# Performance work log

Measured on AMD Instinct MI355X. Metric: run time of the kernel, lower is better.

## Reference

```python
import jax, jax.numpy as jnp
import numpy as np

L = 3          # num_layer
D = 128        # emb_dim
N_INST = 40000
N_NET = 10000
N = N_INST + N_NET
E = 800000
EPS = 1e-5


def setup_inputs() -> dict:
    key = jax.random.key(0)
    ks = jax.random.split(key, 16)
    g = lambda k, shape: jax.random.normal(k, shape, jnp.float32) * 0.05
    return {
        'x': jax.random.normal(ks[0], (N_INST, 11), jnp.float32),
        'x_net': jax.random.normal(ks[1], (N_NET, 3), jnp.float32),
        # encoder for instance nodes: 11 -> 2D -> D
        'enc_W1': g(ks[2], (2 * D, 11)), 'enc_b1': jnp.zeros((2 * D,), jnp.float32),
        'enc_W2': g(ks[3], (D, 2 * D)), 'enc_b2': jnp.zeros((D,), jnp.float32),
        # encoder for net nodes: 3 -> D -> D
        'encn_W1': g(ks[4], (D, 3)), 'encn_b1': jnp.zeros((D,), jnp.float32),
        'encn_W2': g(ks[5], (D, D)), 'encn_b2': jnp.zeros((D,), jnp.float32),
        # forward-direction GCN convs
        'conv_W': g(ks[6], (L, D, D)), 'conv_b': jnp.zeros((L, D), jnp.float32),
        'conv_root': g(ks[7], (L, D)),
        # reverse-direction GCN convs
        'rconv_W': g(ks[8], (L, D, D)), 'rconv_b': jnp.zeros((L, D), jnp.float32),
        'rconv_root': g(ks[9], (L, D)),
        # layernorms
        'ln_g': jnp.ones((L, D), jnp.float32), 'ln_b': jnp.zeros((L, D), jnp.float32),
        # graph edge list
        'src': jax.random.randint(ks[10], (E,), 0, N, jnp.int32),
        'dst': jax.random.randint(ks[11], (E,), 0, N, jnp.int32),
        'num_instances': N_INST,
    }


def _lrelu(v):
    return jnp.where(v >= 0, v, 0.1 * v)


def _gcn_conv(h, W, b, root, e_src, e_dst, deg, dinv):
    # h: [N, D]; e_src/e_dst: [E]; deg/dinv: [N]
    x = h @ W.T + b                                   # [N, D]
    norm = dinv[e_src] * dinv[e_dst]                  # [E]
    msg = norm[:, None] * jax.nn.relu(x[e_src])       # [E, D] gather + scale
    agg = jax.ops.segment_sum(msg, e_dst, num_segments=N)  # [N, D] scatter-add
    self_loop = jax.nn.relu(x + root) / deg[:, None]
    return agg + self_loop


def reference(x, x_net, enc_W1, enc_b1, enc_W2, enc_b2,
              encn_W1, encn_b1, encn_W2, encn_b2,
              conv_W, conv_b, conv_root, rconv_W, rconv_b, rconv_root,
              ln_g, ln_b, src, dst, num_instances):
    # node encoders
    h_inst = _lrelu(_lrelu(x @ enc_W1.T + enc_b1) @ enc_W2.T + enc_b2)
    h_net = _lrelu(_lrelu(x_net @ encn_W1.T + encn_b1) @ encn_W2.T + encn_b2)
    h = jnp.concatenate([h_inst, h_net], axis=0)      # [N, D]

    ones = jnp.ones((E,), jnp.float32)
    deg_in = jax.ops.segment_sum(ones, dst, num_segments=N) + 1.0
    deg_out = jax.ops.segment_sum(ones, src, num_segments=N) + 1.0
    dinv_in = jnp.where(jnp.isinf(deg_in ** -0.5), 0.0, deg_in ** -0.5)
    dinv_out = jnp.where(jnp.isinf(deg_out ** -0.5), 0.0, deg_out ** -0.5)

    h_list = [h]
    for l in range(L):
        hf = _gcn_conv(h, conv_W[l], conv_b[l], conv_root[l], src, dst, deg_in, dinv_in)
        # reverse graph: edges flipped -> src/dst swapped, degrees swap roles
        hr = _gcn_conv(h, rconv_W[l], rconv_b[l], rconv_root[l], dst, src, deg_out, dinv_out)
        s = hf + hr
        mu = jnp.mean(s, axis=-1, keepdims=True)
        var = jnp.mean((s - mu) ** 2, axis=-1, keepdims=True)
        s = (s - mu) * jax.lax.rsqrt(var + EPS) * ln_g[l] + ln_b[l]
        s = _lrelu(s)
        h = s + h  # residual
        h_list.append(h)

    rep = jnp.concatenate(h_list, axis=1)             # [N, (L+1)*D] (JK='concat')
    return rep[num_instances:]                        # net-node representations
```

## Files before the change

kernel.cpp:

```cpp
#include <hip/hip_runtime.h>
#include <hip/hip_bf16.h>


constexpr int D = 128;
constexpr int CAP = 48;

typedef float f32x4 __attribute__((ext_vector_type(4)));
typedef float f32x2 __attribute__((ext_vector_type(2)));
typedef __bf16 bf16x8v __attribute__((ext_vector_type(8)));

#if defined(__has_builtin)
# if __has_builtin(__builtin_amdgcn_cvt_pk_f32_fp8) && __has_builtin(__builtin_amdgcn_cvt_pk_fp8_f32)
#  define HAS_HW_FP8 1
# endif
#endif
#ifndef HAS_HW_FP8
# define HAS_HW_FP8 0
#endif

__device__ __forceinline__ unsigned short f2bf(float f) {
    unsigned u = __float_as_uint(f);
    unsigned r = (u + 0x7fffu + ((u >> 16) & 1u)) >> 16;
    return (unsigned short)r;
}
__device__ __forceinline__ float bflo(unsigned u) { return __uint_as_float(u << 16); }
__device__ __forceinline__ float bfhi(unsigned u) { return __uint_as_float(u & 0xffff0000u); }

__device__ __forceinline__ unsigned enc_fp8_1(float f) {
    unsigned u = __float_as_uint(f);
    u += 0x7FFFFu + ((u >> 20) & 1u);
    int e = (int)(u >> 23) - 120;
    unsigned m = (u >> 20) & 7u;
    if (e <= 0) return 0u;
    if (e > 15 || (e == 15 && m == 7u)) return 0x7Eu;
    return ((unsigned)e << 3) | m;
}
__device__ __forceinline__ unsigned pack_fp8x2(float a, float b) {
#if HAS_HW_FP8
    return (unsigned)__builtin_amdgcn_cvt_pk_fp8_f32(a, b, 0, false) & 0xFFFFu;
#else
    return enc_fp8_1(a) | (enc_fp8_1(b) << 8);
#endif
}
__device__ __forceinline__ float dec_fp8_1(unsigned b) {
    unsigned e = (b >> 3) & 0xFu, m = b & 7u;
    unsigned bits = ((e + 120u) << 23) | (m << 20);
    return e ? __uint_as_float(bits) : 0.0f;
}
__device__ __forceinline__ void dec_fp8x4(unsigned u, float o[4]) {
#if HAS_HW_FP8
    f32x2 lo = __builtin_amdgcn_cvt_pk_f32_fp8((int)u, false);
    f32x2 hi = __builtin_amdgcn_cvt_pk_f32_fp8((int)u, true);
    o[0] = lo.x; o[1] = lo.y; o[2] = hi.x; o[3] = hi.y;
#else
    o[0] = dec_fp8_1(u & 0xFF); o[1] = dec_fp8_1((u >> 8) & 0xFF);
    o[2] = dec_fp8_1((u >> 16) & 0xFF); o[3] = dec_fp8_1(u >> 24);
#endif
}

__global__ __launch_bounds__(256) void prep_kernel(
    const float* __restrict__ cW, const float* __restrict__ rW,
    const float* __restrict__ eW2, const float* __restrict__ enW2,
    unsigned short* __restrict__ cWb, unsigned short* __restrict__ rWb,
    unsigned short* __restrict__ eW2b, unsigned short* __restrict__ enW2b,
    int* __restrict__ cnt_i, int* __restrict__ cnt_o,
    int ncw, int nrw, int new2, int nenw2, int N)
{
    int i = blockIdx.x * 256 + threadIdx.x;
    if (i < ncw) { cWb[i] = f2bf(cW[i]); return; }
    i -= ncw;
    if (i < nrw) { rWb[i] = f2bf(rW[i]); return; }
    i -= nrw;
    if (i < new2) { eW2b[i] = f2bf(eW2[i]); return; }
    i -= new2;
    if (i < nenw2) { enW2b[i] = f2bf(enW2[i]); return; }
    i -= nenw2;
    if (i < N) { cnt_i[i] = 0; return; }
    i -= N;
    if (i < N) { cnt_o[i] = 0; }
}

__global__ __launch_bounds__(256) void fill_part(
    const int* __restrict__ src, const int* __restrict__ dst, int E,
    int* __restrict__ cnt_i, int* __restrict__ cnt_o,
    unsigned short* __restrict__ slot_i, unsigned short* __restrict__ slot_o,
    int N, int prange, int chunk)
{
    int part = blockIdx.x & 7;
    int slice = blockIdx.x >> 3;
    int lo = part * prange, hi = min(N, lo + prange);
    int e0 = slice * chunk, e1 = min(E, e0 + chunk);
    for (int e = e0 + (int)threadIdx.x * 4; e < e1; e += 1024) {
        int4 s4 = *(const int4*)(src + e);
        int4 d4 = *(const int4*)(dst + e);
        int ss[4] = {s4.x, s4.y, s4.z, s4.w};
        int dd[4] = {d4.x, d4.y, d4.z, d4.w};
        #pragma unroll
        for (int j = 0; j < 4; ++j) {
            int d = dd[j], s = ss[j];
            if (d >= lo && d < hi) {
                int p = atomicAdd(&cnt_i[d], 1);
                if (p < CAP) slot_i[(size_t)d * CAP + p] = (unsigned short)s;
            }
            if (s >= lo && s < hi) {
                int p = atomicAdd(&cnt_o[s], 1);
                if (p < CAP) slot_o[(size_t)s * CAP + p] = (unsigned short)d;
            }
        }
    }
}

__global__ __launch_bounds__(256) void enc_gemm1(
    const float* __restrict__ x, const float* __restrict__ x_net,
    const float* __restrict__ W1, const float* __restrict__ b1,
    const float* __restrict__ Wn1, const float* __restrict__ bn1,
    unsigned short* __restrict__ t1, unsigned short* __restrict__ t2,
    int NI, int NN, int nbi)
{
    int b = blockIdx.x;
    const float *A, *W, *bias; unsigned short* Cb;
    int M, K, OUT, ldc, bx, by;
    if (b < nbi * 4) {
        bx = b >> 2; by = b & 3;
        A = x; W = W1; bias = b1; Cb = t1; M = NI; K = 11; OUT = 256; ldc = 256;
    } else {
        b -= nbi * 4;
        bx = b >> 1; by = b & 1;
        A = x_net; W = Wn1; bias = bn1; Cb = t2; M = NN; K = 3; OUT = 128; ldc = 128;
    }
    __shared__ __align__(16) float As[16][68];
    __shared__ __align__(16) float Ws[16][68];
    int row0 = bx * 64, col0 = by * 64;
    int t = threadIdx.x;
    int tx = t & 15, ty = t >> 4;
    float acc[4][4] = {};
    {
        #pragma unroll
        for (int i = 0; i < 4; ++i) {
            int e = t + i * 256;
            int m = e >> 4, k = e & 15;
            int gr = row0 + m;
            As[k][m] = (gr < M && k < K) ? A[(size_t)gr * K + k] : 0.f;
            int gn = col0 + m;
            Ws[k][m] = (gn < OUT && k < K) ? W[(size_t)gn * K + k] : 0.f;
        }
        __syncthreads();
        #pragma unroll
        for (int k = 0; k < 16; ++k) {
            float4 av = *(const float4*)&As[k][ty * 4];
            float4 bv = *(const float4*)&Ws[k][tx * 4];
            float a[4] = {av.x, av.y, av.z, av.w};
            float bb[4] = {bv.x, bv.y, bv.z, bv.w};
            #pragma unroll
            for (int ii = 0; ii < 4; ++ii)
                #pragma unroll
                for (int jj = 0; jj < 4; ++jj)
                    acc[ii][jj] = fmaf(a[ii], bb[jj], acc[ii][jj]);
        }
    }
    #pragma unroll
    for (int ii = 0; ii < 4; ++ii) {
        int gr = row0 + ty * 4 + ii;
        if (gr >= M) continue;
        #pragma unroll
        for (int jj = 0; jj < 4; ++jj) {
            int gn = col0 + tx * 4 + jj;
            if (gn >= OUT) continue;
            float v = acc[ii][jj] + bias[gn];
            v = (v >= 0.f) ? v : 0.1f * v;
            Cb[(size_t)gr * ldc + gn] = f2bf(v);
        }
    }
}

__device__ __forceinline__ void mfma_core(
    const unsigned short* __restrict__ A, const unsigned short* __restrict__ W,
    int M, int K, int row0, int lane, f32x4 acc[8])
{
    int arc = min(row0 + (lane & 15), M - 1);
    int kq = (lane >> 4) * 8;
    const unsigned short* arow = A + (size_t)arc * K + kq;
    const unsigned short* wbase = W + (size_t)(lane & 15) * K + kq;
    for (int k0 = 0; k0 < K; k0 += 32) {
        bf16x8v a = *reinterpret_cast<const bf16x8v*>(arow + k0);
        #pragma unroll
        for (int j = 0; j < 8; ++j) {
            bf16x8v b = *reinterpret_cast<const bf16x8v*>(wbase + (size_t)j * 16 * K + k0);
            acc[j] = __builtin_amdgcn_mfma_f32_16x16x32_bf16(a, b, acc[j], 0, 0, 0);
        }
    }
}

__global__ __launch_bounds__(256) void enc_gemm2(
    const unsigned short* __restrict__ t1, const unsigned short* __restrict__ t2,
    const unsigned short* __restrict__ W2b, const unsigned short* __restrict__ Wn2b,
    const float* __restrict__ b2, const float* __restrict__ bn2,
    float* __restrict__ h, unsigned short* __restrict__ hb,
    float* __restrict__ out, int NI, int NN, int nbi)
{
    int b = blockIdx.x;
    const unsigned short *A, *W; const float* bias;
    int M, K; bool isnet;
    int wave = threadIdx.x >> 6;
    int lane = threadIdx.x & 63;
    int row0;
    if (b < nbi) {
        A = t1; W = W2b; bias = b2; M = NI; K = 256; isnet = false;
        row0 = b * 64 + wave * 16;
    } else {
        A = t2; W = Wn2b; bias = bn2; M = NN; K = 128; isnet = true;
        row0 = (b - nbi) * 64 + wave * 16;
    }
    f32x4 acc[8];
    #pragma unroll
    for (int j = 0; j < 8; ++j) acc[j] = (f32x4){0.f, 0.f, 0.f, 0.f};
    mfma_core(A, W, M, K, row0, lane, acc);
    int cbase = lane & 15;
    int rsub = (lane >> 4) * 4;
    #pragma unroll
    for (int j = 0; j < 8; ++j) {
        int f = j * 16 + cbase;
        float bv = bias[f];
        #pragma unroll
        for (int q = 0; q < 4; ++q) {
            int r = row0 + rsub + q;
            if (r >= M) continue;
            float v = acc[j][q] + bv;
            v = (v >= 0.f) ? v : 0.1f * v;
            int gr = isnet ? NI + r : r;
            h[(size_t)gr * D + f] = v;
            hb[(size_t)gr * D + f] = f2bf(v);
            if (isnet) out[(size_t)r * 512 + f] = v;
        }
    }
}

__global__ __launch_bounds__(256) void conv_gemm(
    const unsigned short* __restrict__ hb,
    const unsigned short* __restrict__ Wf, const unsigned short* __restrict__ Wr,
    const float* __restrict__ biasf, const float* __restrict__ biasr,
    const float* __restrict__ rootf, const float* __restrict__ rootr,
    const int* __restrict__ cnt_i, const int* __restrict__ cnt_o,
    unsigned char* __restrict__ mf, unsigned char* __restrict__ mr,
    unsigned short* __restrict__ sl, int M)
{
    int wave = threadIdx.x >> 6;
    int lane = threadIdx.x & 63;
    int row0 = blockIdx.x * 64 + wave * 16;
    f32x4 accf[8], accr[8];
    #pragma unroll
    for (int j = 0; j < 8; ++j) {
        accf[j] = (f32x4){0.f, 0.f, 0.f, 0.f};
        accr[j] = (f32x4){0.f, 0.f, 0.f, 0.f};
    }
    int arc = min(row0 + (lane & 15), M - 1);
    int kq = (lane >> 4) * 8;
    const unsigned short* arow = hb + (size_t)arc * D + kq;
    const unsigned short* wfb = Wf + (size_t)(lane & 15) * D + kq;
    const unsigned short* wrb = Wr + (size_t)(lane & 15) * D + kq;
    for (int k0 = 0; k0 < D; k0 += 32) {
        bf16x8v a = *reinterpret_cast<const bf16x8v*>(arow + k0);
        #pragma unroll
        for (int j = 0; j < 8; ++j) {
            bf16x8v bf_ = *reinterpret_cast<const bf16x8v*>(wfb + (size_t)j * 16 * D + k0);
            accf[j] = __builtin_amdgcn_mfma_f32_16x16x32_bf16(a, bf_, accf[j], 0, 0, 0);
        }
        #pragma unroll
        for (int j = 0; j < 8; ++j) {
            bf16x8v br_ = *reinterpret_cast<const bf16x8v*>(wrb + (size_t)j * 16 * D + k0);
            accr[j] = __builtin_amdgcn_mfma_f32_16x16x32_bf16(a, br_, accr[j], 0, 0, 0);
        }
    }
    int cbase = lane & 15;
    int rsub = (lane >> 4) * 4;
    float di[4], dou[4], rdi[4], rdo[4];
    #pragma unroll
    for (int q = 0; q < 4; ++q) {
        int r = min(row0 + rsub + q, M - 1);
        float ci = (float)cnt_i[r] + 1.0f;
        float co = (float)cnt_o[r] + 1.0f;
        di[q] = rsqrtf(ci) * 64.0f; rdi[q] = 1.0f / ci;
        dou[q] = rsqrtf(co) * 64.0f; rdo[q] = 1.0f / co;
    }
    #pragma unroll
    for (int j = 0; j < 8; j += 2) {
        int f0 = j * 16 + cbase, f1 = f0 + 16;
        float bf0 = biasf[f0], bf1 = biasf[f1];
        float br0 = biasr[f0], br1 = biasr[f1];
        float rf0 = rootf[f0], rf1 = rootf[f1];
        float rr0 = rootr[f0], rr1 = rootr[f1];
        #pragma unroll
        for (int q = 0; q < 4; ++q) {
            int r = row0 + rsub + q;
            if (r >= M) continue;
            float vf0 = accf[j][q] + bf0, vf1 = accf[j + 1][q] + bf1;
            float vr0 = accr[j][q] + br0, vr1 = accr[j + 1][q] + br1;
            size_t o0 = (size_t)r * D + f0, o1 = (size_t)r * D + f1;
            unsigned em = pack_fp8x2(di[q] * fmaxf(vf0, 0.f), di[q] * fmaxf(vf1, 0.f));
            mf[o0] = (unsigned char)(em & 0xFF);
            mf[o1] = (unsigned char)(em >> 8);
            unsigned er = pack_fp8x2(dou[q] * fmaxf(vr0, 0.f), dou[q] * fmaxf(vr1, 0.f));
            mr[o0] = (unsigned char)(er & 0xFF);
            mr[o1] = (unsigned char)(er >> 8);
            sl[o0] = f2bf(fmaxf(vf0 + rf0, 0.f) * rdi[q] + fmaxf(vr0 + rr0, 0.f) * rdo[q]);
            sl[o1] = f2bf(fmaxf(vf1 + rf1, 0.f) * rdi[q] + fmaxf(vr1 + rr1, 0.f) * rdo[q]);
        }
    }
}

__device__ __forceinline__ void gather_dir(
    const unsigned char* __restrict__ m, const unsigned short* __restrict__ lst,
    int sn, int lane, int rl, size_t fb, float a[4])
{
    int idx = (lane < sn) ? (int)lst[lane] : 0;
    int k = 0;
    for (; k + 8 <= sn; k += 8) {
        int p0 = __shfl(idx, k + rl);
        int p1 = __shfl(idx, k + 2 + rl);
        int p2 = __shfl(idx, k + 4 + rl);
        int p3 = __shfl(idx, k + 6 + rl);
        unsigned u0 = *(const unsigned*)(m + (((size_t)p0) << 7) + fb);
        unsigned u1 = *(const unsigned*)(m + (((size_t)p1) << 7) + fb);
        unsigned u2 = *(const unsigned*)(m + (((size_t)p2) << 7) + fb);
        unsigned u3 = *(const unsigned*)(m + (((size_t)p3) << 7) + fb);
        float t0[4], t1[4], t2[4], t3[4];
        dec_fp8x4(u0, t0); dec_fp8x4(u1, t1); dec_fp8x4(u2, t2); dec_fp8x4(u3, t3);
        a[0] += t0[0] + t1[0] + t2[0] + t3[0];
        a[1] += t0[1] + t1[1] + t2[1] + t3[1];
        a[2] += t0[2] + t1[2] + t2[2] + t3[2];
        a[3] += t0[3] + t1[3] + t2[3] + t3[3];
    }
    for (; k + 2 <= sn; k += 2) {
        int p = __shfl(idx, k + rl);
        unsigned u = *(const unsigned*)(m + (((size_t)p) << 7) + fb);
        float t[4];
        dec_fp8x4(u, t);
        a[0] += t[0]; a[1] += t[1]; a[2] += t[2]; a[3] += t[3];
    }
    if (k < sn) {
        int p = __shfl(idx, k);
        if (rl == 0) {
            unsigned u = *(const unsigned*)(m + (((size_t)p) << 7) + fb);
            float t[4];
            dec_fp8x4(u, t);
            a[0] += t[0]; a[1] += t[1]; a[2] += t[2]; a[3] += t[3];
        }
    }
}

__global__ __launch_bounds__(256) void agg_kernel(
    const unsigned char* __restrict__ mf, const unsigned char* __restrict__ mr,
    const unsigned short* __restrict__ sl,
    float* __restrict__ h, unsigned short* __restrict__ hb,
    const int* __restrict__ cnt_i, const unsigned short* __restrict__ slot_i,
    const int* __restrict__ cnt_o, const unsigned short* __restrict__ slot_o,
    const float* __restrict__ g, const float* __restrict__ bta,
    float* __restrict__ out, int N, int NI, int layer)
{
    int wid = (blockIdx.x * blockDim.x + threadIdx.x) >> 6;
    if (wid >= N) return;
    int lane = threadIdx.x & 63;
    int fl = lane & 31;
    int rl = lane >> 5;
    size_t fb = (size_t)fl * 4;

    int ci_raw = cnt_i[wid], co_raw = cnt_o[wid];
    int sni = min(ci_raw, CAP), sno = min(co_raw, CAP);

    float a[4] = {0.f, 0.f, 0.f, 0.f};
    float b[4] = {0.f, 0.f, 0.f, 0.f};
    gather_dir(mf, slot_i + (size_t)wid * CAP, sni, lane, rl, fb, a);
    gather_dir(mr, slot_o + (size_t)wid * CAP, sno, lane, rl, fb, b);

    #pragma unroll
    for (int j = 0; j < 4; ++j) {
        a[j] += __shfl_xor(a[j], 32);
        b[j] += __shfl_xor(b[j], 32);
    }
    int half = lane >> 1;
    float ta0 = __shfl(a[0], half), ta1 = __shfl(a[1], half);
    float ta2 = __shfl(a[2], half), ta3 = __shfl(a[3], half);
    float tb0 = __shfl(b[0], half), tb1 = __shfl(b[1], half);
    float tb2 = __shfl(b[2], half), tb3 = __shfl(b[3], half);
    float ga0 = (lane & 1) ? ta2 : ta0;
    float ga1 = (lane & 1) ? ta3 : ta1;
    float gb0 = (lane & 1) ? tb2 : tb0;
    float gb1 = (lane & 1) ? tb3 : tb1;

    int d0 = lane * 2;
    float di = rsqrtf((float)ci_raw + 1.0f) * 0.015625f;
    float dou = rsqrtf((float)co_raw + 1.0f) * 0.015625f;
    unsigned usl = *(const unsigned*)(sl + (((size_t)wid) << 7) + d0);
    float s_0 = di * ga0 + dou * gb0 + bflo(usl);
    float s_1 = di * ga1 + dou * gb1 + bfhi(usl);

    float sm = s_0 + s_1;
    float sq = s_0 * s_0 + s_1 * s_1;
    #pragma unroll
    for (int o = 32; o >= 1; o >>= 1) {
        sm += __shfl_xor(sm, o);
        sq += __shfl_xor(sq, o);
    }
    float mu = sm * (1.0f / 128.0f);
    float var = sq * (1.0f / 128.0f) - mu * mu;
    float rs = rsqrtf(var + 1e-5f);

    float2 gv = *(const float2*)(g + d0);
    float2 bv = *(const float2*)(bta + d0);
    float2 hv = *(const float2*)(h + (((size_t)wid) << 7) + d0);
    float y0 = (s_0 - mu) * rs * gv.x + bv.x;
    float y1 = (s_1 - mu) * rs * gv.y + bv.y;
    y0 = (y0 >= 0.f) ? y0 : 0.1f * y0;
    y1 = (y1 >= 0.f) ? y1 : 0.1f * y1;
    y0 += hv.x; y1 += hv.y;
    *(float2*)(h + (((size_t)wid) << 7) + d0) = make_float2(y0, y1);
    if (layer < 2) {
        unsigned packed = (unsigned)f2bf(y0) | ((unsigned)f2bf(y1) << 16);
        *(unsigned*)(hb + (((size_t)wid) << 7) + d0) = packed;
    }
    if (wid >= NI) {
        *(float2*)(out + (size_t)(wid - NI) * 512 + (size_t)(layer + 1) * 128 + d0) = make_float2(y0, y1);
    }
}

static inline int cdiv(int a, int b) { return (a + b - 1) / b; }

extern "C" void kernel_launch(void* const* d_in, const int* in_sizes, int n_in,
                              void* d_out, int out_size, void* d_ws, size_t ws_size,
                              hipStream_t stream)
{
    const float* x        = (const float*)d_in[0];
    const float* x_net    = (const float*)d_in[1];
    const float* enc_W1   = (const float*)d_in[2];
    const float* enc_b1   = (const float*)d_in[3];
    const float* enc_W2   = (const float*)d_in[4];
    const float* enc_b2   = (const float*)d_in[5];
    const float* encn_W1  = (const float*)d_in[6];
    const float* encn_b1  = (const float*)d_in[7];
    const float* encn_W2  = (const float*)d_in[8];
    const float* encn_b2  = (const float*)d_in[9];
    const float* conv_W   = (const float*)d_in[10];
    const float* conv_b   = (const float*)d_in[11];
    const float* conv_root= (const float*)d_in[12];
    const float* rconv_W  = (const float*)d_in[13];
    const float* rconv_b  = (const float*)d_in[14];
    const float* rconv_root=(const float*)d_in[15];
    const float* ln_g     = (const float*)d_in[16];
    const float* ln_b     = (const float*)d_in[17];
    const int*   src      = (const int*)d_in[18];
    const int*   dst      = (const int*)d_in[19];

    const int NI = in_sizes[0] / 11;
    const int NN = in_sizes[1] / 3;
    const int N  = NI + NN;
    const int E  = in_sizes[18];
    float* out = (float*)d_out;

    char* ws = (char*)d_ws;
    size_t offq = 0;
    auto alloc = [&](size_t bytes) -> void* {
        void* p = ws + offq;
        offq += (bytes + 255) & ~(size_t)255;
        return p;
    };
    float*          h    = (float*)alloc((size_t)N * D * 4);
    unsigned short* hb   = (unsigned short*)alloc((size_t)N * D * 2);
    unsigned char*  mf   = (unsigned char*)alloc((size_t)N * D);
    unsigned char*  mr   = (unsigned char*)alloc((size_t)N * D);
    unsigned short* sl   = (unsigned short*)alloc((size_t)N * D * 2);
    unsigned short* tmp2b = (unsigned short*)alloc((size_t)NN * D * 2);
    unsigned short* slot_i = (unsigned short*)alloc((size_t)N * CAP * 2);
    unsigned short* slot_o = (unsigned short*)alloc((size_t)N * CAP * 2);
    int*   cnt_i  = (int*)alloc((size_t)N * 4);
    int*   cnt_o  = (int*)alloc((size_t)N * 4);
    unsigned short* encW2b  = (unsigned short*)alloc((size_t)in_sizes[4] * 2);
    unsigned short* encnW2b = (unsigned short*)alloc((size_t)in_sizes[8] * 2);
    unsigned short* convWb  = (unsigned short*)alloc((size_t)in_sizes[10] * 2);
    unsigned short* rconvWb = (unsigned short*)alloc((size_t)in_sizes[13] * 2);
    unsigned short* tmp1b = (unsigned short*)mf;

    const int ncw = in_sizes[10], nrw = in_sizes[13];
    const int new2 = in_sizes[4], nenw2 = in_sizes[8];
    int prep_total = ncw + nrw + new2 + nenw2 + 2 * N;
    prep_kernel<<<cdiv(prep_total, 256), 256, 0, stream>>>(
        conv_W, rconv_W, enc_W2, encn_W2, convWb, rconvWb, encW2b, encnW2b,
        cnt_i, cnt_o, ncw, nrw, new2, nenw2, N);

    const int prange = cdiv(N, 8);
    const int chunk = 4096;
    const int NS = cdiv(E, chunk);
    fill_part<<<8 * NS, 256, 0, stream>>>(src, dst, E, cnt_i, cnt_o,
                                          slot_i, slot_o, N, prange, chunk);

    const int nbi1 = cdiv(NI, 64);
    const int nbn1 = cdiv(NN, 64);
    enc_gemm1<<<nbi1 * 4 + nbn1 * 2, 256, 0, stream>>>(
        x, x_net, enc_W1, enc_b1, encn_W1, encn_b1, tmp1b, tmp2b, NI, NN, nbi1);
    enc_gemm2<<<nbi1 + nbn1, 256, 0, stream>>>(
        tmp1b, tmp2b, encW2b, encnW2b, enc_b2, encn_b2, h, hb, out, NI, NN, nbi1);

    for (int l = 0; l < 3; ++l) {
        conv_gemm<<<cdiv(N, 64), 256, 0, stream>>>(
            hb, convWb + (size_t)l * D * D, rconvWb + (size_t)l * D * D,
            conv_b + (size_t)l * D, rconv_b + (size_t)l * D,
            conv_root + (size_t)l * D, rconv_root + (size_t)l * D,
            cnt_i, cnt_o, mf, mr, sl, N);
        agg_kernel<<<cdiv(N * 64, 256), 256, 0, stream>>>(
            mf, mr, sl, h, hb, cnt_i, slot_i, cnt_o, slot_o,
            ln_g + (size_t)l * D, ln_b + (size_t)l * D,
            out, N, NI, l);
    }
}
```

Measured before the change: 413.0 us.

## Fuse all stages into one cooperative persistent kernel with grid syncs

Replaces the sequence of separate kernel launches (prep, fill, two encoder GEMMs, per-layer conv and aggregation) with a single cooperative persistent kernel that loops over tiles and separates stages with grid-wide syncs. The aim is to remove launch gaps and tail effects between the many short stages. The conv GEMM tile also changes to 32 rows, with waves split across column halves, and fp8 packing becomes per-element. The cost is grid-sync overhead, occupancy limits from the 256x4 launch bounds, and fill/encoder work now sharing one phase. A fallback path with separate launches is kept.

```diff
diff --git a/kernel.cpp b/kernel.cpp
--- a/kernel.cpp
+++ b/kernel.cpp
@@ -1,5 +1,8 @@
 #include <hip/hip_runtime.h>
 #include <hip/hip_bf16.h>
+#include <hip/hip_cooperative_groups.h>
+
+namespace cg = cooperative_groups;
 
 
 constexpr int D = 128;
@@ -35,11 +38,11 @@
     if (e > 15 || (e == 15 && m == 7u)) return 0x7Eu;
     return ((unsigned)e << 3) | m;
 }
-__device__ __forceinline__ unsigned pack_fp8x2(float a, float b) {
+__device__ __forceinline__ unsigned enc_fp8(float a) {
 #if HAS_HW_FP8
-    return (unsigned)__builtin_amdgcn_cvt_pk_fp8_f32(a, b, 0, false) & 0xFFFFu;
+    return (unsigned)__builtin_amdgcn_cvt_pk_fp8_f32(a, 0.f, 0, false) & 0xFFu;
 #else
-    return enc_fp8_1(a) | (enc_fp8_1(b) << 8);
+    return enc_fp8_1(a);
 #endif
 }
 __device__ __forceinline__ float dec_fp8_1(unsigned b) {
@@ -58,97 +61,115 @@
 #endif
 }
 
-__global__ __launch_bounds__(256) void prep_kernel(
-    const float* __restrict__ cW, const float* __restrict__ rW,
-    const float* __restrict__ eW2, const float* __restrict__ enW2,
-    unsigned short* __restrict__ cWb, unsigned short* __restrict__ rWb,
-    unsigned short* __restrict__ eW2b, unsigned short* __restrict__ enW2b,
-    int* __restrict__ cnt_i, int* __restrict__ cnt_o,
-    int ncw, int nrw, int new2, int nenw2, int N)
-{
-    int i = blockIdx.x * 256 + threadIdx.x;
-    if (i < ncw) { cWb[i] = f2bf(cW[i]); return; }
-    i -= ncw;
-    if (i < nrw) { rWb[i] = f2bf(rW[i]); return; }
-    i -= nrw;
-    if (i < new2) { eW2b[i] = f2bf(eW2[i]); return; }
-    i -= new2;
-    if (i < nenw2) { enW2b[i] = f2bf(enW2[i]); return; }
-    i -= nenw2;
-    if (i < N) { cnt_i[i] = 0; return; }
-    i -= N;
-    if (i < N) { cnt_o[i] = 0; }
-}
-
-__global__ __launch_bounds__(256) void fill_part(
-    const int* __restrict__ src, const int* __restrict__ dst, int E,
-    int* __restrict__ cnt_i, int* __restrict__ cnt_o,
-    unsigned short* __restrict__ slot_i, unsigned short* __restrict__ slot_o,
-    int N, int prange, int chunk)
-{
-    int part = blockIdx.x & 7;
-    int slice = blockIdx.x >> 3;
-    int lo = part * prange, hi = min(N, lo + prange);
-    int e0 = slice * chunk, e1 = min(E, e0 + chunk);
-    for (int e = e0 + (int)threadIdx.x * 4; e < e1; e += 1024) {
-        int4 s4 = *(const int4*)(src + e);
-        int4 d4 = *(const int4*)(dst + e);
+struct MegaParams {
+    const float *x, *x_net;
+    const float *enc_W1, *enc_b1, *enc_b2;
+    const float *encn_W1, *encn_b1, *encn_b2;
+    const float *conv_W, *conv_b, *conv_root;
+    const float *rconv_W, *rconv_b, *rconv_root;
+    const float *ln_g, *ln_b;
+    const float *enc_W2, *encn_W2;
+    const int *src, *dst;
+    float* h; unsigned short* hb;
+    unsigned char *mf, *mr; unsigned short* sl;
+    unsigned short *t1, *t2;
+    unsigned short *slot_i, *slot_o;
+    int *cnt_i, *cnt_o;
+    unsigned short *cWb, *rWb, *eW2b, *enW2b;
+    float* out;
+    int NI, NN, N, E;
+    int ncw, nrw, new2, nenw2;
+    int nbi1, nbn1, nb;
+};
+
+
+__device__ __forceinline__ void body_prep(const MegaParams& P, int bid, int nb)
+{
+    int tid = threadIdx.x;
+    int total = P.ncw + P.nrw + P.new2 + P.nenw2 + 2 * P.N;
+    for (int idx = bid * 256 + tid; idx < total; idx += nb * 256) {
+        int i = idx;
+        if (i < P.ncw) { P.cWb[i] = f2bf(P.conv_W[i]); continue; }
+        i -= P.ncw;
+        if (i < P.nrw) { P.rWb[i] = f2bf(P.rconv_W[i]); continue; }
+        i -= P.nrw;
+        if (i < P.new2) { P.eW2b[i] = f2bf(P.enc_W2[i]); continue; }
+        i -= P.new2;
+        if (i < P.nenw2) { P.enW2b[i] = f2bf(P.encn_W2[i]); continue; }
+        i -= P.nenw2;
+        if (i < P.N) { P.cnt_i[i] = 0; continue; }
+        i -= P.N;
+        P.cnt_o[i] = 0;
+    }
+}
+
+__device__ __forceinline__ void body_fill(const MegaParams& P, int bid, int nb)
+{
+    int tid = threadIdx.x;
+    int part = bid & 7, slice = bid >> 3;
+    int slices = nb >> 3;
+    int chunk = ((P.E + slices - 1) / slices + 3) & ~3;
+    int prange = (P.N + 7) >> 3;
+    int lo = part * prange, hi = min(P.N, lo + prange);
+    int e0 = slice * chunk, e1 = min(P.E, e0 + chunk);
+    for (int e = e0 + tid * 4; e < e1; e += 1024) {
+        int4 s4 = *(const int4*)(P.src + e);
+        int4 d4 = *(const int4*)(P.dst + e);
         int ss[4] = {s4.x, s4.y, s4.z, s4.w};
         int dd[4] = {d4.x, d4.y, d4.z, d4.w};
         #pragma unroll
         for (int j = 0; j < 4; ++j) {
             int d = dd[j], s = ss[j];
             if (d >= lo && d < hi) {
-                int p = atomicAdd(&cnt_i[d], 1);
-                if (p < CAP) slot_i[(size_t)d * CAP + p] = (unsigned short)s;
+                int p = atomicAdd(&P.cnt_i[d], 1);
+                if (p < CAP) P.slot_i[(size_t)d * CAP + p] = (unsigned short)s;
             }
             if (s >= lo && s < hi) {
-                int p = atomicAdd(&cnt_o[s], 1);
-                if (p < CAP) slot_o[(size_t)s * CAP + p] = (unsigned short)d;
-            }
-        }
-    }
-}
-
-__global__ __launch_bounds__(256) void enc_gemm1(
-    const float* __restrict__ x, const float* __restrict__ x_net,
-    const float* __restrict__ W1, const float* __restrict__ b1,
-    const float* __restrict__ Wn1, const float* __restrict__ bn1,
-    unsigned short* __restrict__ t1, unsigned short* __restrict__ t2,
-    int NI, int NN, int nbi)
-{
-    int b = blockIdx.x;
-    const float *A, *W, *bias; unsigned short* Cb;
-    int M, K, OUT, ldc, bx, by;
-    if (b < nbi * 4) {
-        bx = b >> 2; by = b & 3;
-        A = x; W = W1; bias = b1; Cb = t1; M = NI; K = 11; OUT = 256; ldc = 256;
-    } else {
-        b -= nbi * 4;
-        bx = b >> 1; by = b & 1;
-        A = x_net; W = Wn1; bias = bn1; Cb = t2; M = NN; K = 3; OUT = 128; ldc = 128;
-    }
-    __shared__ __align__(16) float As[16][68];
-    __shared__ __align__(16) float Ws[16][68];
-    int row0 = bx * 64, col0 = by * 64;
-    int t = threadIdx.x;
-    int tx = t & 15, ty = t >> 4;
-    float acc[4][4] = {};
-    {
+                int p = atomicAdd(&P.cnt_o[s], 1);
+                if (p < CAP) P.slot_o[(size_t)s * CAP + p] = (unsigned short)d;
+            }
+        }
+    }
+}
+
+__device__ __forceinline__ void body_enc1(const MegaParams& P, int bid, int nb)
+{
+    __shared__ __align__(16) float s_As[16][68];
+    __shared__ __align__(16) float s_Ws[16][68];
+    int tid = threadIdx.x;
+    int ntile = P.nbi1 * 4 + P.nbn1 * 2;
+    for (int t = bid; t < ntile; t += nb) {
+        __syncthreads();
+        int b = t;
+        const float *A, *W, *bias; unsigned short* Cb;
+        int M, K, OUT, ldc, bx, by;
+        if (b < P.nbi1 * 4) {
+            bx = b >> 2; by = b & 3;
+            A = P.x; W = P.enc_W1; bias = P.enc_b1; Cb = P.t1;
+            M = P.NI; K = 11; OUT = 256; ldc = 256;
+        } else {
+            b -= P.nbi1 * 4;
+            bx = b >> 1; by = b & 1;
+            A = P.x_net; W = P.encn_W1; bias = P.encn_b1; Cb = P.t2;
+            M = P.NN; K = 3; OUT = 128; ldc = 128;
+        }
+        int row0 = bx * 64, col0 = by * 64;
+        int tx = tid & 15, ty = tid >> 4;
+        float acc[4][4] = {};
         #pragma unroll
         for (int i = 0; i < 4; ++i) {
-            int e = t + i * 256;
+            int e = tid + i * 256;
             int m = e >> 4, k = e & 15;
             int gr = row0 + m;
-            As[k][m] = (gr < M && k < K) ? A[(size_t)gr * K + k] : 0.f;
+            s_As[k][m] = (gr < M && k < K) ? A[(size_t)gr * K + k] : 0.f;
             int gn = col0 + m;
-            Ws[k][m] = (gn < OUT && k < K) ? W[(size_t)gn * K + k] : 0.f;
+            s_Ws[k][m] = (gn < OUT && k < K) ? W[(size_t)gn * K + k] : 0.f;
         }
         __syncthreads();
         #pragma unroll
         for (int k = 0; k < 16; ++k) {
-            float4 av = *(const float4*)&As[k][ty * 4];
-            float4 bv = *(const float4*)&Ws[k][tx * 4];
+            float4 av = *(const float4*)&s_As[k][ty * 4];
+            float4 bv = *(const float4*)&s_Ws[k][tx * 4];
             float a[4] = {av.x, av.y, av.z, av.w};
             float bb[4] = {bv.x, bv.y, bv.z, bv.w};
             #pragma unroll
@@ -157,163 +178,144 @@
                 for (int jj = 0; jj < 4; ++jj)
                     acc[ii][jj] = fmaf(a[ii], bb[jj], acc[ii][jj]);
         }
-    }
-    #pragma unroll
-    for (int ii = 0; ii < 4; ++ii) {
-        int gr = row0 + ty * 4 + ii;
-        if (gr >= M) continue;
-        #pragma unroll
-        for (int jj = 0; jj < 4; ++jj) {
-            int gn = col0 + tx * 4 + jj;
-            if (gn >= OUT) continue;
-            float v = acc[ii][jj] + bias[gn];
-            v = (v >= 0.f) ? v : 0.1f * v;
-            Cb[(size_t)gr * ldc + gn] = f2bf(v);
-        }
-    }
-}
-
-__device__ __forceinline__ void mfma_core(
-    const unsigned short* __restrict__ A, const unsigned short* __restrict__ W,
-    int M, int K, int row0, int lane, f32x4 acc[8])
-{
-    int arc = min(row0 + (lane & 15), M - 1);
-    int kq = (lane >> 4) * 8;
-    const unsigned short* arow = A + (size_t)arc * K + kq;
-    const unsigned short* wbase = W + (size_t)(lane & 15) * K + kq;
-    for (int k0 = 0; k0 < K; k0 += 32) {
-        bf16x8v a = *reinterpret_cast<const bf16x8v*>(arow + k0);
+        #pragma unroll
+        for (int ii = 0; ii < 4; ++ii) {
+            int gr = row0 + ty * 4 + ii;
+            if (gr >= M) continue;
+            #pragma unroll
+            for (int jj = 0; jj < 4; ++jj) {
+                int gn = col0 + tx * 4 + jj;
+                if (gn >= OUT) continue;
+                float v = acc[ii][jj] + bias[gn];
+                v = (v >= 0.f) ? v : 0.1f * v;
+                Cb[(size_t)gr * ldc + gn] = f2bf(v);
+            }
+        }
+    }
+}
+
+__device__ __forceinline__ void body_enc2(const MegaParams& P, int bid, int nb)
+{
+    int wave = threadIdx.x >> 6, lane = threadIdx.x & 63;
+    int ntile = P.nbi1 + P.nbn1;
+    for (int t = bid; t < ntile; t += nb) {
+        const unsigned short *A, *W; const float* bias;
+        int M, K; bool isnet; int row0;
+        if (t < P.nbi1) {
+            A = P.t1; W = P.eW2b; bias = P.enc_b2; M = P.NI; K = 256; isnet = false;
+            row0 = t * 64 + wave * 16;
+        } else {
+            A = P.t2; W = P.enW2b; bias = P.encn_b2; M = P.NN; K = 128; isnet = true;
+            row0 = (t - P.nbi1) * 64 + wave * 16;
+        }
+        f32x4 acc[8];
+        #pragma unroll
+        for (int j = 0; j < 8; ++j) acc[j] = (f32x4){0.f, 0.f, 0.f, 0.f};
+        int arc = min(row0 + (lane & 15), M - 1);
+        int kq = (lane >> 4) * 8;
+        const unsigned short* arow = A + (size_t)arc * K + kq;
+        const unsigned short* wbase = W + (size_t)(lane & 15) * K + kq;
+        for (int k0 = 0; k0 < K; k0 += 32) {
+            bf16x8v a = *reinterpret_cast<const bf16x8v*>(arow + k0);
+            #pragma unroll
+            for (int j = 0; j < 8; ++j) {
+                bf16x8v b = *reinterpret_cast<const bf16x8v*>(wbase + (size_t)j * 16 * K + k0);
+                acc[j] = __builtin_amdgcn_mfma_f32_16x16x32_bf16(a, b, acc[j], 0, 0, 0);
+            }
+        }
+        int cbase = lane & 15;
+        int rsub = (lane >> 4) * 4;
         #pragma unroll
         for (int j = 0; j < 8; ++j) {
-            bf16x8v b = *reinterpret_cast<const bf16x8v*>(wbase + (size_t)j * 16 * K + k0);
-            acc[j] = __builtin_amdgcn_mfma_f32_16x16x32_bf16(a, b, acc[j], 0, 0, 0);
-        }
-    }
-}
-
-__global__ __launch_bounds__(256) void enc_gemm2(
-    const unsigned short* __restrict__ t1, const unsigned short* __restrict__ t2,
-    const unsigned short* __restrict__ W2b, const unsigned short* __restrict__ Wn2b,
-    const float* __restrict__ b2, const float* __restrict__ bn2,
-    float* __restrict__ h, unsigned short* __restrict__ hb,
-    float* __restrict__ out, int NI, int NN, int nbi)
-{
-    int b = blockIdx.x;
-    const unsigned short *A, *W; const float* bias;
-    int M, K; bool isnet;
-    int wave = threadIdx.x >> 6;
-    int lane = threadIdx.x & 63;
-    int row0;
-    if (b < nbi) {
-        A = t1; W = W2b; bias = b2; M = NI; K = 256; isnet = false;
-        row0 = b * 64 + wave * 16;
-    } else {
-        A = t2; W = Wn2b; bias = bn2; M = NN; K = 128; isnet = true;
-        row0 = (b - nbi) * 64 + wave * 16;
-    }
-    f32x4 acc[8];
-    #pragma unroll
-    for (int j = 0; j < 8; ++j) acc[j] = (f32x4){0.f, 0.f, 0.f, 0.f};
-    mfma_core(A, W, M, K, row0, lane, acc);
+            int f = j * 16 + cbase;
+            float bv = bias[f];
+            #pragma unroll
+            for (int q = 0; q < 4; ++q) {
+                int r = row0 + rsub + q;
+                if (r >= M) continue;
+                float v = acc[j][q] + bv;
+                v = (v >= 0.f) ? v : 0.1f * v;
+                int gr = isnet ? P.NI + r : r;
+                P.h[(size_t)gr * D + f] = v;
+                P.hb[(size_t)gr * D + f] = f2bf(v);
+                if (isnet) P.out[(size_t)r * 512 + f] = v;
+            }
+        }
+    }
+}
+
+__device__ __forceinline__ void body_conv(const MegaParams& P, int l, int bid, int nb)
+{
+    const unsigned short* Wf = P.cWb + (size_t)l * D * D;
+    const unsigned short* Wr = P.rWb + (size_t)l * D * D;
+    const float* biasf = P.conv_b + (size_t)l * D;
+    const float* biasr = P.rconv_b + (size_t)l * D;
+    const float* rootf = P.conv_root + (size_t)l * D;
+    const float* rootr = P.rconv_root + (size_t)l * D;
+    int wave = threadIdx.x >> 6, lane = threadIdx.x & 63;
+    int ntc = (P.N + 31) >> 5;
+    int rg = wave >> 1, cgp = wave & 1;
     int cbase = lane & 15;
     int rsub = (lane >> 4) * 4;
-    #pragma unroll
-    for (int j = 0; j < 8; ++j) {
-        int f = j * 16 + cbase;
-        float bv = bias[f];
+    int kq = (lane >> 4) * 8;
+    for (int t = bid; t < ntc; t += nb) {
+        int row0 = t * 32 + rg * 16;
+        f32x4 accf[4], accr[4];
+        #pragma unroll
+        for (int j = 0; j < 4; ++j) {
+            accf[j] = (f32x4){0.f, 0.f, 0.f, 0.f};
+            accr[j] = (f32x4){0.f, 0.f, 0.f, 0.f};
+        }
+        int arc = min(row0 + cbase, P.N - 1);
+        const unsigned short* arow = P.hb + (size_t)arc * D + kq;
+        const unsigned short* wfb = Wf + (size_t)(cgp * 64 + cbase) * D + kq;
+        const unsigned short* wrb = Wr + (size_t)(cgp * 64 + cbase) * D + kq;
+        for (int k0 = 0; k0 < D; k0 += 32) {
+            bf16x8v a = *reinterpret_cast<const bf16x8v*>(arow + k0);
+            #pragma unroll
+            for (int j = 0; j < 4; ++j) {
+                bf16x8v bf_ = *reinterpret_cast<const bf16x8v*>(wfb + (size_t)j * 16 * D + k0);
+                accf[j] = __builtin_amdgcn_mfma_f32_16x16x32_bf16(a, bf_, accf[j], 0, 0, 0);
+            }
+            #pragma unroll
+            for (int j = 0; j < 4; ++j) {
+                bf16x8v br_ = *reinterpret_cast<const bf16x8v*>(wrb + (size_t)j * 16 * D + k0);
+                accr[j] = __builtin_amdgcn_mfma_f32_16x16x32_bf16(a, br_, accr[j], 0, 0, 0);
+            }
+        }
+        float di[4], dou[4], rdi[4], rdo[4];
         #pragma unroll
         for (int q = 0; q < 4; ++q) {
-            int r = row0 + rsub + q;
-            if (r >= M) continue;
-            float v = acc[j][q] + bv;
-            v = (v >= 0.f) ? v : 0.1f * v;
-            int gr = isnet ? NI + r : r;
-            h[(size_t)gr * D + f] = v;
-            hb[(size_t)gr * D + f] = f2bf(v);
-            if (isnet) out[(size_t)r * 512 + f] = v;
-        }
-    }
-}
-
-__global__ __launch_bounds__(256) void conv_gemm(
-    const unsigned short* __restrict__ hb,
-    const unsigned short* __restrict__ Wf, const unsigned short* __restrict__ Wr,
-    const float* __restrict__ biasf, const float* __restrict__ biasr,
-    const float* __restrict__ rootf, const float* __restrict__ rootr,
-    const int* __restrict__ cnt_i, const int* __restrict__ cnt_o,
-    unsigned char* __restrict__ mf, unsigned char* __restrict__ mr,
-    unsigned short* __restrict__ sl, int M)
-{
-    int wave = threadIdx.x >> 6;
-    int lane = threadIdx.x & 63;
-    int row0 = blockIdx.x * 64 + wave * 16;
-    f32x4 accf[8], accr[8];
-    #pragma unroll
-    for (int j = 0; j < 8; ++j) {
-        accf[j] = (f32x4){0.f, 0.f, 0.f, 0.f};
-        accr[j] = (f32x4){0.f, 0.f, 0.f, 0.f};
-    }
-    int arc = min(row0 + (lane & 15), M - 1);
-    int kq = (lane >> 4) * 8;
-    const unsigned short* arow = hb + (size_t)arc * D + kq;
-    const unsigned short* wfb = Wf + (size_t)(lane & 15) * D + kq;
-    const unsigned short* wrb = Wr + (size_t)(lane & 15) * D + kq;
-    for (int k0 = 0; k0 < D; k0 += 32) {
-        bf16x8v a = *reinterpret_cast<const bf16x8v*>(arow + k0);
-        #pragma unroll
-        for (int j = 0; j < 8; ++j) {
-            bf16x8v bf_ = *reinterpret_cast<const bf16x8v*>(wfb + (size_t)j * 16 * D + k0);
-            accf[j] = __builtin_amdgcn_mfma_f32_16x16x32_bf16(a, bf_, accf[j], 0, 0, 0);
-        }
-        #pragma unroll
-        for (int j = 0; j < 8; ++j) {
-            bf16x8v br_ = *reinterpret_cast<const bf16x8v*>(wrb + (size_t)j * 16 * D + k0);
-            accr[j] = __builtin_amdgcn_mfma_f32_16x16x32_bf16(a, br_, accr[j], 0, 0, 0);
-        }
-    }
-    int cbase = lane & 15;
-    int rsub = (lane >> 4) * 4;
-    float di[4], dou[4], rdi[4], rdo[4];
-    #pragma unroll
-    for (int q = 0; q < 4; ++q) {
-        int r = min(row0 + rsub + q, M - 1);
-        float ci = (float)cnt_i[r] + 1.0f;
-        float co = (float)cnt_o[r] + 1.0f;
-        di[q] = rsqrtf(ci) * 64.0f; rdi[q] = 1.0f / ci;
-        dou[q] = rsqrtf(co) * 64.0f; rdo[q] = 1.0f / co;
-    }
-    #pragma unroll
-    for (int j = 0; j < 8; j += 2) {
-        int f0 = j * 16 + cbase, f1 = f0 + 16;
-        float bf0 = biasf[f0], bf1 = biasf[f1];
-        float br0 = biasr[f0], br1 = biasr[f1];
-        float rf0 = rootf[f0], rf1 = rootf[f1];
-        float rr0 = rootr[f0], rr1 = rootr[f1];
-        #pragma unroll
-        for (int q = 0; q < 4; ++q) {
-            int r = row0 + rsub + q;
-            if (r >= M) continue;
-            float vf0 = accf[j][q] + bf0, vf1 = accf[j + 1][q] + bf1;
-            float vr0 = accr[j][q] + br0, vr1 = accr[j + 1][q] + br1;
-            size_t o0 = (size_t)r * D + f0, o1 = (size_t)r * D + f1;
-            unsigned em = pack_fp8x2(di[q] * fmaxf(vf0, 0.f), di[q] * fmaxf(vf1, 0.f));
-            mf[o0] = (unsigned char)(em & 0xFF);
-            mf[o1] = (unsigned char)(em >> 8);
-            unsigned er = pack_fp8x2(dou[q] * fmaxf(vr0, 0.f), dou[q] * fmaxf(vr1, 0.f));
-            mr[o0] = (unsigned char)(er & 0xFF);
-            mr[o1] = (unsigned char)(er >> 8);
-            sl[o0] = f2bf(fmaxf(vf0 + rf0, 0.f) * rdi[q] + fmaxf(vr0 + rr0, 0.f) * rdo[q]);
-            sl[o1] = f2bf(fmaxf(vf1 + rf1, 0.f) * rdi[q] + fmaxf(vr1 + rr1, 0.f) * rdo[q]);
-        }
-    }
-}
-
-__device__ __forceinline__ void gather_dir(
-    const unsigned char* __restrict__ m, const unsigned short* __restrict__ lst,
-    int sn, int lane, int rl, size_t fb, float a[4])
-{
-    int idx = (lane < sn) ? (int)lst[lane] : 0;
-    int k = 0;
+            int r = min(row0 + rsub + q, P.N - 1);
+            float ci = (float)P.cnt_i[r] + 1.0f;
+            float co = (float)P.cnt_o[r] + 1.0f;
+            di[q] = rsqrtf(ci) * 64.0f; rdi[q] = 1.0f / ci;
+            dou[q] = rsqrtf(co) * 64.0f; rdo[q] = 1.0f / co;
+        }
+        #pragma unroll
+        for (int j = 0; j < 4; ++j) {
+            int f = cgp * 64 + j * 16 + cbase;
+            float bfv = biasf[f], brv = biasr[f];
+            float rfv = rootf[f], rrv = rootr[f];
+            #pragma unroll
+            for (int q = 0; q < 4; ++q) {
+                int r = row0 + rsub + q;
+                if (r >= P.N) continue;
+                float vf = accf[j][q] + bfv;
+                float vr = accr[j][q] + brv;
+                size_t o = (size_t)r * D + f;
+                P.mf[o] = (unsigned char)enc_fp8(di[q] * fmaxf(vf, 0.f));
+                P.mr[o] = (unsigned char)enc_fp8(dou[q] * fmaxf(vr, 0.f));
+                P.sl[o] = f2bf(fmaxf(vf + rfv, 0.f) * rdi[q] + fmaxf(vr + rrv, 0.f) * rdo[q]);
+            }
+        }
+    }
+}
+
+__device__ __forceinline__ void gather_tail(
+    const unsigned char* __restrict__ m, int idx, int k, int sn,
+    int rl, size_t fb, float a[4])
+{
     for (; k + 8 <= sn; k += 8) {
         int p0 = __shfl(idx, k + rl);
         int p1 = __shfl(idx, k + 2 + rl);
@@ -323,12 +325,12 @@
         unsigned u1 = *(const unsigned*)(m + (((size_t)p1) << 7) + fb);
         unsigned u2 = *(const unsigned*)(m + (((size_t)p2) << 7) + fb);
         unsigned u3 = *(const unsigned*)(m + (((size_t)p3) << 7) + fb);
-        float t0[4], t1[4], t2[4], t3[4];
-        dec_fp8x4(u0, t0); dec_fp8x4(u1, t1); dec_fp8x4(u2, t2); dec_fp8x4(u3, t3);
-        a[0] += t0[0] + t1[0] + t2[0] + t3[0];
-        a[1] += t0[1] + t1[1] + t2[1] + t3[1];
-        a[2] += t0[2] + t1[2] + t2[2] + t3[2];
-        a[3] += t0[3] + t1[3] + t2[3] + t3[3];
+        float t0[4], t1_[4], t2_[4], t3[4];
+        dec_fp8x4(u0, t0); dec_fp8x4(u1, t1_); dec_fp8x4(u2, t2_); dec_fp8x4(u3, t3);
+        a[0] += t0[0] + t1_[0] + t2_[0] + t3[0];
+        a[1] += t0[1] + t1_[1] + t2_[1] + t3[1];
+        a[2] += t0[2] + t1_[2] + t2_[2] + t3[2];
+        a[3] += t0[3] + t1_[3] + t2_[3] + t3[3];
     }
     for (; k + 2 <= sn; k += 2) {
         int p = __shfl(idx, k + rl);
@@ -348,80 +350,131 @@
     }
 }
 
-__global__ __launch_bounds__(256) void agg_kernel(
-    const unsigned char* __restrict__ mf, const unsigned char* __restrict__ mr,
-    const unsigned short* __restrict__ sl,
-    float* __restrict__ h, unsigned short* __restrict__ hb,
-    const int* __restrict__ cnt_i, const unsigned short* __restrict__ slot_i,
-    const int* __restrict__ cnt_o, const unsigned short* __restrict__ slot_o,
-    const float* __restrict__ g, const float* __restrict__ bta,
-    float* __restrict__ out, int N, int NI, int layer)
-{
-    int wid = (blockIdx.x * blockDim.x + threadIdx.x) >> 6;
-    if (wid >= N) return;
-    int lane = threadIdx.x & 63;
+__device__ __forceinline__ void body_agg(const MegaParams& P, int l, int bid, int nb)
+{
+    int wave = threadIdx.x >> 6, lane = threadIdx.x & 63;
     int fl = lane & 31;
     int rl = lane >> 5;
     size_t fb = (size_t)fl * 4;
-
-    int ci_raw = cnt_i[wid], co_raw = cnt_o[wid];
-    int sni = min(ci_raw, CAP), sno = min(co_raw, CAP);
-
-    float a[4] = {0.f, 0.f, 0.f, 0.f};
-    float b[4] = {0.f, 0.f, 0.f, 0.f};
-    gather_dir(mf, slot_i + (size_t)wid * CAP, sni, lane, rl, fb, a);
-    gather_dir(mr, slot_o + (size_t)wid * CAP, sno, lane, rl, fb, b);
-
-    #pragma unroll
-    for (int j = 0; j < 4; ++j) {
-        a[j] += __shfl_xor(a[j], 32);
-        b[j] += __shfl_xor(b[j], 32);
-    }
-    int half = lane >> 1;
-    float ta0 = __shfl(a[0], half), ta1 = __shfl(a[1], half);
-    float ta2 = __shfl(a[2], half), ta3 = __shfl(a[3], half);
-    float tb0 = __shfl(b[0], half), tb1 = __shfl(b[1], half);
-    float tb2 = __shfl(b[2], half), tb3 = __shfl(b[3], half);
-    float ga0 = (lane & 1) ? ta2 : ta0;
-    float ga1 = (lane & 1) ? ta3 : ta1;
-    float gb0 = (lane & 1) ? tb2 : tb0;
-    float gb1 = (lane & 1) ? tb3 : tb1;
-
-    int d0 = lane * 2;
-    float di = rsqrtf((float)ci_raw + 1.0f) * 0.015625f;
-    float dou = rsqrtf((float)co_raw + 1.0f) * 0.015625f;
-    unsigned usl = *(const unsigned*)(sl + (((size_t)wid) << 7) + d0);
-    float s_0 = di * ga0 + dou * gb0 + bflo(usl);
-    float s_1 = di * ga1 + dou * gb1 + bfhi(usl);
-
-    float sm = s_0 + s_1;
-    float sq = s_0 * s_0 + s_1 * s_1;
-    #pragma unroll
-    for (int o = 32; o >= 1; o >>= 1) {
-        sm += __shfl_xor(sm, o);
-        sq += __shfl_xor(sq, o);
-    }
-    float mu = sm * (1.0f / 128.0f);
-    float var = sq * (1.0f / 128.0f) - mu * mu;
-    float rs = rsqrtf(var + 1e-5f);
-
-    float2 gv = *(const float2*)(g + d0);
-    float2 bv = *(const float2*)(bta + d0);
-    float2 hv = *(const float2*)(h + (((size_t)wid) << 7) + d0);
-    float y0 = (s_0 - mu) * rs * gv.x + bv.x;
-    float y1 = (s_1 - mu) * rs * gv.y + bv.y;
-    y0 = (y0 >= 0.f) ? y0 : 0.1f * y0;
-    y1 = (y1 >= 0.f) ? y1 : 0.1f * y1;
-    y0 += hv.x; y1 += hv.y;
-    *(float2*)(h + (((size_t)wid) << 7) + d0) = make_float2(y0, y1);
-    if (layer < 2) {
-        unsigned packed = (unsigned)f2bf(y0) | ((unsigned)f2bf(y1) << 16);
-        *(unsigned*)(hb + (((size_t)wid) << 7) + d0) = packed;
-    }
-    if (wid >= NI) {
-        *(float2*)(out + (size_t)(wid - NI) * 512 + (size_t)(layer + 1) * 128 + d0) = make_float2(y0, y1);
-    }
-}
+    for (int wid = bid * 4 + wave; wid < P.N; wid += nb * 4) {
+        int vi = P.cnt_i[wid], vo = P.cnt_o[wid];
+        int sni = min(vi, CAP), sno = min(vo, CAP);
+        float degi = (float)vi + 1.0f, dego = (float)vo + 1.0f;
+
+        int idxA = (lane < sni) ? (int)P.slot_i[(size_t)wid * CAP + lane] : 0;
+        int idxB = (lane < sno) ? (int)P.slot_o[(size_t)wid * CAP + lane] : 0;
+
+        float a[4] = {0.f, 0.f, 0.f, 0.f};
+        float b[4] = {0.f, 0.f, 0.f, 0.f};
+        int k = 0;
+        while (k + 8 <= sni && k + 8 <= sno) {
+            int pA0 = __shfl(idxA, k + rl);
+            int pA1 = __shfl(idxA, k + 2 + rl);
+            int pA2 = __shfl(idxA, k + 4 + rl);
+            int pA3 = __shfl(idxA, k + 6 + rl);
+            int pB0 = __shfl(idxB, k + rl);
+            int pB1 = __shfl(idxB, k + 2 + rl);
+            int pB2 = __shfl(idxB, k + 4 + rl);
+            int pB3 = __shfl(idxB, k + 6 + rl);
+            unsigned uA0 = *(const unsigned*)(P.mf + (((size_t)pA0) << 7) + fb);
+            unsigned uA1 = *(const unsigned*)(P.mf + (((size_t)pA1) << 7) + fb);
+            unsigned uA2 = *(const unsigned*)(P.mf + (((size_t)pA2) << 7) + fb);
+            unsigned uA3 = *(const unsigned*)(P.mf + (((size_t)pA3) << 7) + fb);
+            unsigned uB0 = *(const unsigned*)(P.mr + (((size_t)pB0) << 7) + fb);
+            unsigned uB1 = *(const unsigned*)(P.mr + (((size_t)pB1) << 7) + fb);
+            unsigned uB2 = *(const unsigned*)(P.mr + (((size_t)pB2) << 7) + fb);
+            unsigned uB3 = *(const unsigned*)(P.mr + (((size_t)pB3) << 7) + fb);
+            float tA0[4], tA1[4], tA2[4], tA3[4], tB0[4], tB1[4], tB2[4], tB3[4];
+            dec_fp8x4(uA0, tA0); dec_fp8x4(uA1, tA1); dec_fp8x4(uA2, tA2); dec_fp8x4(uA3, tA3);
+            dec_fp8x4(uB0, tB0); dec_fp8x4(uB1, tB1); dec_fp8x4(uB2, tB2); dec_fp8x4(uB3, tB3);
+            #pragma unroll
+            for (int j = 0; j < 4; ++j) {
+                a[j] += tA0[j] + tA1[j] + tA2[j] + tA3[j];
+                b[j] += tB0[j] + tB1[j] + tB2[j] + tB3[j];
+            }
+            k += 8;
+        }
+        gather_tail(P.mf, idxA, k, sni, rl, fb, a);
+        gather_tail(P.mr, idxB, k, sno, rl, fb, b);
+
+        #pragma unroll
+        for (int j = 0; j < 4; ++j) {
+            a[j] += __shfl_xor(a[j], 32);
+            b[j] += __shfl_xor(b[j], 32);
+        }
+        int half = lane >> 1;
+        float ta0 = __shfl(a[0], half), ta1 = __shfl(a[1], half);
+        float ta2 = __shfl(a[2], half), ta3 = __shfl(a[3], half);
+        float tb0 = __shfl(b[0], half), tb1 = __shfl(b[1], half);
+        float tb2 = __shfl(b[2], half), tb3 = __shfl(b[3], half);
+        float ga0 = (lane & 1) ? ta2 : ta0;
+        float ga1 = (lane & 1) ? ta3 : ta1;
+        float gb0 = (lane & 1) ? tb2 : tb0;
+        float gb1 = (lane & 1) ? tb3 : tb1;
+
+        int d0 = lane * 2;
+        float dsi = rsqrtf(degi) * 0.015625f;
+        float dso = rsqrtf(dego) * 0.015625f;
+        unsigned usl = *(const unsigned*)(P.sl + (((size_t)wid) << 7) + d0);
+        float s_0 = dsi * ga0 + dso * gb0 + bflo(usl);
+        float s_1 = dsi * ga1 + dso * gb1 + bfhi(usl);
+
+        float sm = s_0 + s_1;
+        float sq = s_0 * s_0 + s_1 * s_1;
+        #pragma unroll
+        for (int o = 32; o >= 1; o >>= 1) {
+            sm += __shfl_xor(sm, o);
+            sq += __shfl_xor(sq, o);
+        }
+        float mu = sm * (1.0f / 128.0f);
+        float var = sq * (1.0f / 128.0f) - mu * mu;
+        float rs = rsqrtf(var + 1e-5f);
+
+        float2 gv = *(const float2*)(P.ln_g + (size_t)l * D + d0);
+        float2 bv = *(const float2*)(P.ln_b + (size_t)l * D + d0);
+        float2 hv = *(const float2*)(P.h + (((size_t)wid) << 7) + d0);
+        float y0 = (s_0 - mu) * rs * gv.x + bv.x;
+        float y1 = (s_1 - mu) * rs * gv.y + bv.y;
+        y0 = (y0 >= 0.f) ? y0 : 0.1f * y0;
+        y1 = (y1 >= 0.f) ? y1 : 0.1f * y1;
+        y0 += hv.x; y1 += hv.y;
+        *(float2*)(P.h + (((size_t)wid) << 7) + d0) = make_float2(y0, y1);
+        if (l < 2) {
+            unsigned packed = (unsigned)f2bf(y0) | ((unsigned)f2bf(y1) << 16);
+            *(unsigned*)(P.hb + (((size_t)wid) << 7) + d0) = packed;
+        }
+        if (wid >= P.NI) {
+            *(float2*)(P.out + (size_t)(wid - P.NI) * 512 + (size_t)(l + 1) * 128 + d0)
+                = make_float2(y0, y1);
+        }
+    }
+}
+
+
+__global__ __launch_bounds__(256, 4) void mega_kernel(MegaParams P)
+{
+    cg::grid_group grid = cg::this_grid();
+    body_prep(P, blockIdx.x, P.nb);
+    grid.sync();
+    body_fill(P, blockIdx.x, P.nb);
+    body_enc1(P, blockIdx.x, P.nb);
+    grid.sync();
+    body_enc2(P, blockIdx.x, P.nb);
+    grid.sync();
+    for (int l = 0; l < 3; ++l) {
+        body_conv(P, l, blockIdx.x, P.nb);
+        grid.sync();
+        body_agg(P, l, blockIdx.x, P.nb);
+        if (l < 2) grid.sync();
+    }
+}
+
+__global__ __launch_bounds__(256) void k_prep(MegaParams P) { body_prep(P, blockIdx.x, gridDim.x); }
+__global__ __launch_bounds__(256) void k_fill(MegaParams P) { body_fill(P, blockIdx.x, gridDim.x); }
+__global__ __launch_bounds__(256) void k_enc1(MegaParams P) { body_enc1(P, blockIdx.x, gridDim.x); }
+__global__ __launch_bounds__(256) void k_enc2(MegaParams P) { body_enc2(P, blockIdx.x, gridDim.x); }
+__global__ __launch_bounds__(256) void k_conv(MegaParams P, int l) { body_conv(P, l, blockIdx.x, gridDim.x); }
+__global__ __launch_bounds__(256) void k_agg(MegaParams P, int l) { body_agg(P, l, blockIdx.x, gridDim.x); }
 
 static inline int cdiv(int a, int b) { return (a + b - 1) / b; }
 
@@ -429,32 +482,33 @@
                               void* d_out, int out_size, void* d_ws, size_t ws_size,
                               hipStream_t stream)
 {
-    const float* x        = (const float*)d_in[0];
-    const float* x_net    = (const float*)d_in[1];
-    const float* enc_W1   = (const float*)d_in[2];
-    const float* enc_b1   = (const float*)d_in[3];
-    const float* enc_W2   = (const float*)d_in[4];
-    const float* enc_b2   = (const float*)d_in[5];
-    const float* encn_W1  = (const float*)d_in[6];
-    const float* encn_b1  = (const float*)d_in[7];
-    const float* encn_W2  = (const float*)d_in[8];
-    const float* encn_b2  = (const float*)d_in[9];
-    const float* conv_W   = (const float*)d_in[10];
-    const float* conv_b   = (const float*)d_in[11];
-    const float* conv_root= (const float*)d_in[12];
-    const float* rconv_W  = (const float*)d_in[13];
-    const float* rconv_b  = (const float*)d_in[14];
-    const float* rconv_root=(const float*)d_in[15];
-    const float* ln_g     = (const float*)d_in[16];
-    const float* ln_b     = (const float*)d_in[17];
-    const int*   src      = (const int*)d_in[18];
-    const int*   dst      = (const int*)d_in[19];
-
-    const int NI = in_sizes[0] / 11;
-    const int NN = in_sizes[1] / 3;
-    const int N  = NI + NN;
-    const int E  = in_sizes[18];
-    float* out = (float*)d_out;
+    MegaParams P;
+    P.x        = (const float*)d_in[0];
+    P.x_net    = (const float*)d_in[1];
+    P.enc_W1   = (const float*)d_in[2];
+    P.enc_b1   = (const float*)d_in[3];
+    P.enc_W2   = (const float*)d_in[4];
+    P.enc_b2   = (const float*)d_in[5];
+    P.encn_W1  = (const float*)d_in[6];
+    P.encn_b1  = (const float*)d_in[7];
+    P.encn_W2  = (const float*)d_in[8];
+    P.encn_b2  = (const float*)d_in[9];
+    P.conv_W   = (const float*)d_in[10];
+    P.conv_b   = (const float*)d_in[11];
+    P.conv_root= (const float*)d_in[12];
+    P.rconv_W  = (const float*)d_in[13];
+    P.rconv_b  = (const float*)d_in[14];
+    P.rconv_root=(const float*)d_in[15];
+    P.ln_g     = (const float*)d_in[16];
+    P.ln_b     = (const float*)d_in[17];
+    P.src      = (const int*)d_in[18];
+    P.dst      = (const int*)d_in[19];
+
+    P.NI = in_sizes[0] / 11;
+    P.NN = in_sizes[1] / 3;
+    P.N  = P.NI + P.NN;
+    P.E  = in_sizes[18];
+    P.out = (float*)d_out;
 
     char* ws = (char*)d_ws;
     size_t offq = 0;
@@ -463,51 +517,53 @@
         offq += (bytes + 255) & ~(size_t)255;
         return p;
     };
-    float*          h    = (float*)alloc((size_t)N * D * 4);
-    unsigned short* hb   = (unsigned short*)alloc((size_t)N * D * 2);
-    unsigned char*  mf   = (unsigned char*)alloc((size_t)N * D);
-    unsigned char*  mr   = (unsigned char*)alloc((size_t)N * D);
-    unsigned short* sl   = (unsigned short*)alloc((size_t)N * D * 2);
-    unsigned short* tmp2b = (unsigned short*)alloc((size_t)NN * D * 2);
-    unsigned short* slot_i = (unsigned short*)alloc((size_t)N * CAP * 2);
-    unsigned short* slot_o = (unsigned short*)alloc((size_t)N * CAP * 2);
-    int*   cnt_i  = (int*)alloc((size_t)N * 4);
-    int*   cnt_o  = (int*)alloc((size_t)N * 4);
-    unsigned short* encW2b  = (unsigned short*)alloc((size_t)in_sizes[4] * 2);
-    unsigned short* encnW2b = (unsigned short*)alloc((size_t)in_sizes[8] * 2);
-    unsigned short* convWb  = (unsigned short*)alloc((size_t)in_sizes[10] * 2);
-    unsigned short* rconvWb = (unsigned short*)alloc((size_t)in_sizes[13] * 2);
-    unsigned short* tmp1b = (unsigned short*)mf;
-
-    const int ncw = in_sizes[10], nrw = in_sizes[13];
-    const int new2 = in_sizes[4], nenw2 = in_sizes[8];
-    int prep_total = ncw + nrw + new2 + nenw2 + 2 * N;
-    prep_kernel<<<cdiv(prep_total, 256), 256, 0, stream>>>(
-        conv_W, rconv_W, enc_W2, encn_W2, convWb, rconvWb, encW2b, encnW2b,
-        cnt_i, cnt_o, ncw, nrw, new2, nenw2, N);
-
-    const int prange = cdiv(N, 8);
-    const int chunk = 4096;
-    const int NS = cdiv(E, chunk);
-    fill_part<<<8 * NS, 256, 0, stream>>>(src, dst, E, cnt_i, cnt_o,
-                                          slot_i, slot_o, N, prange, chunk);
-
-    const int nbi1 = cdiv(NI, 64);
-    const int nbn1 = cdiv(NN, 64);
-    enc_gemm1<<<nbi1 * 4 + nbn1 * 2, 256, 0, stream>>>(
-        x, x_net, enc_W1, enc_b1, encn_W1, encn_b1, tmp1b, tmp2b, NI, NN, nbi1);
-    enc_gemm2<<<nbi1 + nbn1, 256, 0, stream>>>(
-        tmp1b, tmp2b, encW2b, encnW2b, enc_b2, encn_b2, h, hb, out, NI, NN, nbi1);
-
-    for (int l = 0; l < 3; ++l) {
-        conv_gemm<<<cdiv(N, 64), 256, 0, stream>>>(
-            hb, convWb + (size_t)l * D * D, rconvWb + (size_t)l * D * D,
-            conv_b + (size_t)l * D, rconv_b + (size_t)l * D,
-            conv_root + (size_t)l * D, rconv_root + (size_t)l * D,
-            cnt_i, cnt_o, mf, mr, sl, N);
-        agg_kernel<<<cdiv(N * 64, 256), 256, 0, stream>>>(
-            mf, mr, sl, h, hb, cnt_i, slot_i, cnt_o, slot_o,
-            ln_g + (size_t)l * D, ln_b + (size_t)l * D,
-            out, N, NI, l);
-    }
-}
+    P.h    = (float*)alloc((size_t)P.N * D * 4);
+    P.hb   = (unsigned short*)alloc((size_t)P.N * D * 2);
+    P.mf   = (unsigned char*)alloc((size_t)P.N * D);
+    P.mr   = (unsigned char*)alloc((size_t)P.N * D);
+    P.sl   = (unsigned short*)alloc((size_t)P.N * D * 2);
+    P.t2   = (unsigned short*)alloc((size_t)P.NN * D * 2);
+    P.slot_i = (unsigned short*)alloc((size_t)P.N * CAP * 2);
+    P.slot_o = (unsigned short*)alloc((size_t)P.N * CAP * 2);
+    P.cnt_i  = (int*)alloc((size_t)P.N * 4);
+    P.cnt_o  = (int*)alloc((size_t)P.N * 4);
+    P.eW2b   = (unsigned short*)alloc((size_t)in_sizes[4] * 2);
+    P.enW2b  = (unsigned short*)alloc((size_t)in_sizes[8] * 2);
+    P.cWb    = (unsigned short*)alloc((size_t)in_sizes[10] * 2);
+    P.rWb    = (unsigned short*)alloc((size_t)in_sizes[13] * 2);
+    P.t1 = (unsigned short*)P.mf;
+
+    P.ncw = in_sizes[10]; P.nrw = in_sizes[13];
+    P.new2 = in_sizes[4]; P.nenw2 = in_sizes[8];
+    P.nbi1 = cdiv(P.NI, 64);
+    P.nbn1 = cdiv(P.NN, 64);
+
+    int bpc = 0;
+    hipError_t occ = hipOccupancyMaxActiveBlocksPerMultiprocessor(
+        &bpc, (const void*)mega_kernel, 256, 0);
+    int nb = (occ == hipSuccess) ? bpc * 256 : 0;
+    if (nb > 2048) nb = 2048;
+    nb &= ~7;
+
+    bool done = false;
+    if (nb >= 8) {
+        P.nb = nb;
+        void* kargs[] = { &P };
+        hipError_t e = hipLaunchCooperativeKernel((void*)mega_kernel, dim3(nb), dim3(256),
+                                                  kargs, 0, stream);
+        if (e == hipSuccess) done = true;
+        else (void)hipGetLastError();
+    }
+    if (!done) {
+        P.nb = 0;
+        int total = P.ncw + P.nrw + P.new2 + P.nenw2 + 2 * P.N;
+        k_prep<<<cdiv(total, 256), 256, 0, stream>>>(P);
+        k_fill<<<8 * 196, 256, 0, stream>>>(P);
+        k_enc1<<<P.nbi1 * 4 + P.nbn1 * 2, 256, 0, stream>>>(P);
+        k_enc2<<<P.nbi1 + P.nbn1, 256, 0, stream>>>(P);
+        for (int l = 0; l < 3; ++l) {
+            k_conv<<<cdiv(P.N, 32), 256, 0, stream>>>(P, l);
+            k_agg<<<cdiv(P.N, 4), 256, 0, stream>>>(P, l);
+        }
+    }
+}
```

Result: slower. 1.172 ms (+183.7%).
